# Kernel tuning notes

Hardware: AMD Instinct MI355X
Metric: run time of the kernel (lower is better)

Reference implementation:

```python
import jax, jax.numpy as jnp
import numpy as np

N = 100000      # nodes
E = 3200000     # edges
F_IN = 128      # num_features
H = 32          # hidden_dim (hard-coded in module)
C = 8           # num_classes
B = 128         # graphs in batch
BN_EPS = 1e-5


def setup_inputs() -> dict:
    key = jax.random.key(0)
    ks = jax.random.split(key, 24)
    s = 0.1
    inp = {
        "x": jax.random.normal(ks[0], (N, F_IN), jnp.float32),
        "edge_index": jax.random.randint(ks[1], (2, E), 0, N, dtype=jnp.int32),
        "batch": jnp.sort(jax.random.randint(ks[2], (N,), 0, B, dtype=jnp.int32)),
        # GINConv layer 0 (F_IN -> H -> H) MLP + BN params
        "w1_0": jax.random.normal(ks[3], (F_IN, H), jnp.float32) * s,
        "b1_0": jnp.zeros((H,), jnp.float32),
        "w2_0": jax.random.normal(ks[4], (H, H), jnp.float32) * s,
        "b2_0": jnp.zeros((H,), jnp.float32),
        "g_0": jnp.ones((H,), jnp.float32),
        "be_0": jnp.zeros((H,), jnp.float32),
        # GINConv layers 1..3 (H -> H -> H), stacked
        "w1s": jax.random.normal(ks[5], (3, H, H), jnp.float32) * s,
        "b1s": jnp.zeros((3, H), jnp.float32),
        "w2s": jax.random.normal(ks[6], (3, H, H), jnp.float32) * s,
        "b2s": jnp.zeros((3, H), jnp.float32),
        "gs": jnp.ones((3, H), jnp.float32),
        "bes": jnp.zeros((3, H), jnp.float32),
        # classifier head
        "fc1_w": jax.random.normal(ks[7], (H, H), jnp.float32) * s,
        "fc1_b": jnp.zeros((H,), jnp.float32),
        "fc2_w": jax.random.normal(ks[8], (H, C), jnp.float32) * s,
        "fc2_b": jnp.zeros((C,), jnp.float32),
    }
    return inp


def _gin_conv(h, src, dst, w1, b1, w2, b2):
    # GINConv with eps=0: MLP((1+eps)*x + sum_{j in N(i)} x_j)
    agg = jax.ops.segment_sum(h[src], dst, num_segments=N)  # scatter-add aggregation
    z = h + agg
    return jnp.maximum(z @ w1 + b1, 0.0) @ w2 + b2


def _batch_norm(h, gamma, beta):
    # BatchNorm1d in training mode: batch stats over node dim, biased variance
    mean = h.mean(axis=0)
    var = jnp.mean(jnp.square(h - mean), axis=0)
    return gamma * (h - mean) * jax.lax.rsqrt(var + BN_EPS) + beta


def reference(x, edge_index, batch, w1_0, b1_0, w2_0, b2_0, g_0, be_0,
              w1s, b1s, w2s, b2s, gs, bes, fc1_w, fc1_b, fc2_w, fc2_b):
    src, dst = edge_index[0], edge_index[1]
    h = _batch_norm(jnp.maximum(_gin_conv(x, src, dst, w1_0, b1_0, w2_0, b2_0), 0.0), g_0, be_0)
    for i in range(3):  # fixed small layer loop
        h = _batch_norm(jnp.maximum(_gin_conv(h, src, dst, w1s[i], b1s[i], w2s[i], b2s[i]), 0.0), gs[i], bes[i])
    # global_mean_pool over batch ids
    counts = jax.ops.segment_sum(jnp.ones((N,), h.dtype), batch, num_segments=B)
    pooled = jax.ops.segment_sum(h, batch, num_segments=B) / jnp.maximum(counts, 1.0)[:, None]
    h = jnp.maximum(pooled @ fc1_w + fc1_b, 0.0)
    # dropout p=0.5 treated as identity (eval-mode determinism)
    logits = h @ fc2_w + fc2_b
    return jax.nn.log_softmax(logits, axis=-1)
```

## Files before the change

### kernel.cpp

```cpp
#include <hip/hip_runtime.h>
#include <hip/hip_bf16.h>

#define NN   100000
#define EE   3200000
#define HH   32
#define BB   128
#define KMAX 96
#define LSTRIDE 97
#define NBKT 256
#define BSPAN 391
#define WSPAN 98
#define QS   25000
#define EBLK 256
#define CHUNK 12500

static constexpr size_t Q_OFF      = 0;
static constexpr size_t AGG_OFF    = 6400000;
static constexpr size_t H_OFF      = 19200000;
static constexpr size_t EPACK_OFF  = 32000000;
static constexpr size_t EPACK2_OFF = 44800000;
static constexpr size_t SRC_OFF    = 57600000;
static constexpr size_t OFF_OFF    = 70400000;
static constexpr size_t HIST_OFF   = 70900000;
static constexpr size_t START_OFF  = 71200000;
static constexpr size_t BBASE_OFF  = 71500000;
static constexpr size_t KB2_OFF    = 71510000;
static constexpr size_t STATS_OFF  = 71530000;
static constexpr size_t POOLED_OFF = 71531024;
static constexpr size_t PCNT_OFF   = 71547408;
static constexpr size_t ZERO_OFF   = STATS_OFF;
static constexpr size_t ZERO_BYTES = 17920;

__global__ __launch_bounds__(256) void hist_kernel(const int* __restrict__ ei,
                                                   int* __restrict__ hist) {
    __shared__ int lh[NBKT];
    int tid = threadIdx.x, blk = blockIdx.x;
    for (int i = tid; i < NBKT; i += 256) lh[i] = 0;
    __syncthreads();
    int e0 = blk * CHUNK;
    for (int e = e0 + tid; e < e0 + CHUNK; e += 256) {
        int d = ei[EE + e];
        atomicAdd(&lh[d / BSPAN], 1);
    }
    __syncthreads();
    for (int i = tid; i < NBKT; i += 256) hist[blk * NBKT + i] = lh[i];
}

__global__ __launch_bounds__(NBKT) void bucket_scan_kernel(const int* __restrict__ hist,
                                                           int* __restrict__ bbase,
                                                           int* __restrict__ start) {
    __shared__ int sm[NBKT];
    int t = threadIdx.x;
    int mine = 0;
    for (int blk = 0; blk < EBLK; blk++) mine += hist[blk * NBKT + t];
    sm[t] = mine;
    __syncthreads();
    for (int off = 1; off < NBKT; off <<= 1) {
        int v = (t >= off) ? sm[t - off] : 0;
        __syncthreads();
        sm[t] += v;
        __syncthreads();
    }
    int base = sm[t] - mine;
    bbase[t] = base;
    if (t == NBKT - 1) bbase[NBKT] = sm[t];
    int run = base;
    for (int blk = 0; blk < EBLK; blk++) {
        start[blk * NBKT + t] = run;
        run += hist[blk * NBKT + t];
    }
}

__global__ __launch_bounds__(256) void scatter_kernel(const int* __restrict__ ei,
                                                      const int* __restrict__ start,
                                                      int* __restrict__ epack) {
    __shared__ int loff[NBKT];
    int tid = threadIdx.x, blk = blockIdx.x;
    for (int i = tid; i < NBKT; i += 256) loff[i] = start[blk * NBKT + i];
    __syncthreads();
    int e0 = blk * CHUNK;
    for (int e = e0 + tid; e < e0 + CHUNK; e += 256) {
        int s = ei[e];
        int d = ei[EE + e];
        int b = d / BSPAN;
        int slot = atomicAdd(&loff[b], 1);
        epack[slot] = s | ((d - b * BSPAN) << 17);
    }
}

__global__ __launch_bounds__(256) void rescatter_kernel(const int* __restrict__ epack,
                                                        const int* __restrict__ bbase,
                                                        int* __restrict__ epack2,
                                                        int* __restrict__ kb2) {
    __shared__ int lh[16];
    __shared__ int lofs[17];
    __shared__ int lrun[16];
    int b = blockIdx.x, tid = threadIdx.x;
    if (tid < 16) lh[tid] = 0;
    __syncthreads();
    int p0 = bbase[b], p1 = bbase[b + 1];
    for (int i = p0 + tid; i < p1; i += 256) {
        int wd = epack[i];
        int key = ((wd >> 17) / WSPAN) * 4 + (wd & 0x1FFFF) / QS;
        atomicAdd(&lh[key], 1);
    }
    __syncthreads();
    if (tid == 0) {
        int run = p0;
        for (int k = 0; k < 16; k++) { lofs[k] = run; run += lh[k]; }
        lofs[16] = run;
    }
    __syncthreads();
    if (tid < 17) kb2[b * 17 + tid] = lofs[tid];
    if (tid < 16) lrun[tid] = lofs[tid];
    __syncthreads();
    for (int i = p0 + tid; i < p1; i += 256) {
        int wd = epack[i];
        int key = ((wd >> 17) / WSPAN) * 4 + (wd & 0x1FFFF) / QS;
        int slot = atomicAdd(&lrun[key], 1);
        epack2[slot] = wd;
    }
}

__global__ __launch_bounds__(256) void csr_compact_kernel(const int* __restrict__ epack2,
                                                          const int* __restrict__ kb2,
                                                          int* __restrict__ off,
                                                          int* __restrict__ srcs) {
    __shared__ int lcnt[WSPAN];
    __shared__ int lbase[WSPAN + 1];
    __shared__ int lcsr[WSPAN * LSTRIDE];
    int blk = blockIdx.x;
    int b = blk >> 2, w = blk & 3;
    int base = b * BSPAN;
    int span = NN - base;
    if (span <= 0) return;
    if (span > BSPAN) span = BSPAN;
    int wstart = w * WSPAN;
    if (wstart >= span) return;
    int wend = min(wstart + WSPAN, span);
    int wn = wend - wstart;
    int tid = threadIdx.x;
    for (int i = tid; i < wn; i += 256) lcnt[i] = 0;
    __syncthreads();
    int p0w = kb2[b * 17 + w * 4], p1w = kb2[b * 17 + w * 4 + 4];
    for (int i = p0w + tid; i < p1w; i += 256) {
        int wd = epack2[i];
        int ld = (wd >> 17) - wstart;
        int slot = atomicAdd(&lcnt[ld], 1);
        if (slot < KMAX) lcsr[ld * LSTRIDE + slot] = wd & 0x1FFFF;
    }
    __syncthreads();
    if (tid == 0) {
        int run = 0;
        for (int i = 0; i < wn; i++) { lbase[i] = run; run += min(lcnt[i], KMAX); }
        lbase[wn] = run;
    }
    __syncthreads();
    for (int i = tid; i < wn; i += 256) off[base + wstart + i] = p0w + lbase[i];
    if (base + wend == NN && tid == 0) off[NN] = p0w + lbase[wn];
    int m = lbase[wn];
    for (int j = tid; j < m; j += 256) {
        int lo = 0, hi = wn - 1;
        while (lo < hi) {
            int mid = (lo + hi + 1) >> 1;
            if (lbase[mid] <= j) lo = mid; else hi = mid - 1;
        }
        srcs[p0w + j] = lcsr[lo * LSTRIDE + (j - lbase[lo])];
    }
}

__device__ __forceinline__ unsigned bf16rn(float f) {
    unsigned b = __float_as_uint(f);
    return (b + 0x7fffu + ((b >> 16) & 1u)) >> 16;
}

__device__ __forceinline__ void acc_row(float* a, uint4 v) {
    a[0] += __uint_as_float(v.x << 16);
    a[1] += __uint_as_float(v.x & 0xffff0000u);
    a[2] += __uint_as_float(v.y << 16);
    a[3] += __uint_as_float(v.y & 0xffff0000u);
    a[4] += __uint_as_float(v.z << 16);
    a[5] += __uint_as_float(v.z & 0xffff0000u);
    a[6] += __uint_as_float(v.w << 16);
    a[7] += __uint_as_float(v.w & 0xffff0000u);
}

template <int FIN>
__global__ __launch_bounds__(256) void proj_kernel(const float* __restrict__ hin,
                                                   const float* __restrict__ w1,
                                                   const float* __restrict__ stats_prev,
                                                   const float* __restrict__ gamma,
                                                   const float* __restrict__ beta,
                                                   uint4* __restrict__ q4) {
    constexpr int JC = FIN / 4;
    __shared__ float sa[32], sc[32];
    __shared__ float part[4 * 64 * 33];
    int tid = threadIdx.x;
    if constexpr (FIN == 32) {
        if (tid < 32) {
            float mean = stats_prev[tid] * (1.0f / NN);
            float var  = fmaxf(stats_prev[32 + tid] * (1.0f / NN) - mean * mean, 0.f);
            float av = gamma[tid] * rsqrtf(var + 1e-5f);
            sa[tid] = av;
            sc[tid] = beta[tid] - mean * av;
        }
        __syncthreads();
    }
    int wv = __builtin_amdgcn_readfirstlane(tid >> 6);
    int ln = tid & 63;
    int n = blockIdx.x * 64 + ln;
    float acc[32];
#pragma unroll
    for (int c = 0; c < 32; c++) acc[c] = 0.f;
    if (n < NN) {
        const float4* h4 = (const float4*)(hin + (size_t)n * FIN + wv * JC);
        float hv[JC];
#pragma unroll
        for (int k = 0; k < JC / 4; k++) {
            float4 v = h4[k];
            hv[4*k] = v.x; hv[4*k+1] = v.y; hv[4*k+2] = v.z; hv[4*k+3] = v.w;
        }
        if constexpr (FIN == 32) {
#pragma unroll
            for (int j = 0; j < JC; j++) hv[j] = fmaf(hv[j], sa[wv * JC + j], sc[wv * JC + j]);
        }
#pragma unroll 4
        for (int j = 0; j < JC; j++) {
            float hvj = hv[j];
            const float* wrow = w1 + (size_t)(wv * JC + j) * 32;
#pragma unroll
            for (int c = 0; c < 32; c++) acc[c] = fmaf(hvj, wrow[c], acc[c]);
        }
    }
    float* my = part + (wv * 64 + ln) * 33;
#pragma unroll
    for (int c = 0; c < 32; c++) my[c] = acc[c];
    __syncthreads();
    int node = tid >> 2, p = tid & 3;
    int n2 = blockIdx.x * 64 + node;
    if (n2 >= NN) return;
    float r[8];
#pragma unroll
    for (int k = 0; k < 8; k++) {
        int c = p * 8 + k;
        r[k] = (part[(0 * 64 + node) * 33 + c] + part[(1 * 64 + node) * 33 + c])
             + (part[(2 * 64 + node) * 33 + c] + part[(3 * 64 + node) * 33 + c]);
    }
    uint4 u;
    u.x = bf16rn(r[0]) | (bf16rn(r[1]) << 16);
    u.y = bf16rn(r[2]) | (bf16rn(r[3]) << 16);
    u.z = bf16rn(r[4]) | (bf16rn(r[5]) << 16);
    u.w = bf16rn(r[6]) | (bf16rn(r[7]) << 16);
    q4[(size_t)n2 * 4 + p] = u;
}

__global__ __launch_bounds__(256) void gather_kernel(const uint4* __restrict__ q4,
                                                     const int* __restrict__ srcs,
                                                     const int* __restrict__ off,
                                                     const float* __restrict__ b1,
                                                     float* __restrict__ agg) {
    int t = blockIdx.x * 256 + threadIdx.x;
    int n = t >> 2;
    if (n >= NN) return;
    int p = t & 3;
    float a[8];
#pragma unroll
    for (int k = 0; k < 8; k++) a[k] = b1[p * 8 + k];
    acc_row(a, q4[(size_t)n * 4 + p]);
    int o0 = off[n];
    int d = off[n + 1] - o0;
    const int* lst = srcs + o0;
    int i = 0;
    for (; i + 8 <= d; i += 8) {
        int s0 = __builtin_nontemporal_load(lst + i);
        int s1 = __builtin_nontemporal_load(lst + i + 1);
        int s2 = __builtin_nontemporal_load(lst + i + 2);
        int s3 = __builtin_nontemporal_load(lst + i + 3);
        int s4 = __builtin_nontemporal_load(lst + i + 4);
        int s5 = __builtin_nontemporal_load(lst + i + 5);
        int s6 = __builtin_nontemporal_load(lst + i + 6);
        int s7 = __builtin_nontemporal_load(lst + i + 7);
        uint4 v0 = q4[(size_t)s0 * 4 + p];
        uint4 v1 = q4[(size_t)s1 * 4 + p];
        uint4 v2 = q4[(size_t)s2 * 4 + p];
        uint4 v3 = q4[(size_t)s3 * 4 + p];
        uint4 v4 = q4[(size_t)s4 * 4 + p];
        uint4 v5 = q4[(size_t)s5 * 4 + p];
        uint4 v6 = q4[(size_t)s6 * 4 + p];
        uint4 v7 = q4[(size_t)s7 * 4 + p];
        acc_row(a, v0); acc_row(a, v1); acc_row(a, v2); acc_row(a, v3);
        acc_row(a, v4); acc_row(a, v5); acc_row(a, v6); acc_row(a, v7);
    }
    for (; i < d; i++) {
        int s = __builtin_nontemporal_load(lst + i);
        acc_row(a, q4[(size_t)s * 4 + p]);
    }
    float4* ar = (float4*)(agg + (size_t)n * 32 + p * 8);
    float4 f0, f1;
    f0.x = a[0]; f0.y = a[1]; f0.z = a[2]; f0.w = a[3];
    f1.x = a[4]; f1.y = a[5]; f1.z = a[6]; f1.w = a[7];
    ar[0] = f0; ar[1] = f1;
}

__global__ __launch_bounds__(256) void mlp_kernel(const float* __restrict__ agg,
                                                  const float* __restrict__ w2,
                                                  const float* __restrict__ b2,
                                                  float* __restrict__ r,
                                                  float* __restrict__ stats) {
    __shared__ float tile[256 * 33];
    __shared__ float ps[8 * 32];
    __shared__ float pq[8 * 32];
    int tid = threadIdx.x;
    int n = blockIdx.x * 256 + tid;
    float rc[32];
    if (n < NN) {
        float u[32];
        const float4* a4 = (const float4*)(agg + (size_t)n * 32);
#pragma unroll
        for (int k = 0; k < 8; k++) {
            float4 v = a4[k];
            u[4*k]   = fmaxf(v.x, 0.f);
            u[4*k+1] = fmaxf(v.y, 0.f);
            u[4*k+2] = fmaxf(v.z, 0.f);
            u[4*k+3] = fmaxf(v.w, 0.f);
        }
#pragma unroll
        for (int c = 0; c < 32; c++) rc[c] = b2[c];
#pragma unroll 4
        for (int j = 0; j < 32; j++) {
            float uj = u[j];
            const float* wrow = w2 + (size_t)j * 32;
#pragma unroll
            for (int c = 0; c < 32; c++) rc[c] = fmaf(uj, wrow[c], rc[c]);
        }
#pragma unroll
        for (int c = 0; c < 32; c++) rc[c] = fmaxf(rc[c], 0.f);
        float4* rr = (float4*)(r + (size_t)n * 32);
#pragma unroll
        for (int k = 0; k < 8; k++) {
            float4 v; v.x = rc[4*k]; v.y = rc[4*k+1]; v.z = rc[4*k+2]; v.w = rc[4*k+3];
            rr[k] = v;
        }
    } else {
#pragma unroll
        for (int c = 0; c < 32; c++) rc[c] = 0.f;
    }
#pragma unroll
    for (int c = 0; c < 32; c++) tile[tid * 33 + c] = rc[c];
    __syncthreads();
    {
        int c = tid & 31, rb = tid >> 5;
        float s = 0.f, sq = 0.f;
        for (int it = 0; it < 32; it++) {
            float v = tile[(rb * 32 + it) * 33 + c];
            s += v; sq += v * v;
        }
        ps[rb * 32 + c] = s; pq[rb * 32 + c] = sq;
    }
    __syncthreads();
    if (tid < 32) {
        float s = 0.f, sq = 0.f;
#pragma unroll
        for (int rb = 0; rb < 8; rb++) { s += ps[rb * 32 + tid]; sq += pq[rb * 32 + tid]; }
        atomicAdd(&stats[tid], s);
        atomicAdd(&stats[32 + tid], sq);
    }
}

#define PR 16
__global__ __launch_bounds__(256) void pool_kernel(const float* __restrict__ h,
                                                   const int* __restrict__ batch,
                                                   float* __restrict__ pooled,
                                                   float* __restrict__ pcnt) {
    int t = blockIdx.x * 256 + threadIdx.x;
    int c = t & 31;
    int g = t >> 5;
    int r0 = g * PR;
    if (r0 >= NN) return;
    int r1 = min(r0 + PR, NN);
    int cur = batch[r0];
    float acc = 0.f, cn = 0.f;
    for (int rr = r0; rr < r1; rr++) {
        int b = batch[rr];
        if (b != cur) {
            atomicAdd(&pooled[cur * 32 + c], acc);
            if (c == 0) atomicAdd(&pcnt[cur], cn);
            acc = 0.f; cn = 0.f; cur = b;
        }
        acc += h[(size_t)rr * 32 + c];
        cn += 1.f;
    }
    atomicAdd(&pooled[cur * 32 + c], acc);
    if (c == 0) atomicAdd(&pcnt[cur], cn);
}

__global__ __launch_bounds__(128) void head_kernel(const float* __restrict__ pooled,
                                                   const float* __restrict__ pcnt,
                                                   const float* __restrict__ stats3,
                                                   const float* __restrict__ g3,
                                                   const float* __restrict__ be3,
                                                   const float* __restrict__ fc1w,
                                                   const float* __restrict__ fc1b,
                                                   const float* __restrict__ fc2w,
                                                   const float* __restrict__ fc2b,
                                                   float* __restrict__ out) {
    __shared__ float sa[32], sc[32];
    int g = threadIdx.x;
    if (g < 32) {
        float mean = stats3[g] * (1.0f / NN);
        float var  = fmaxf(stats3[32 + g] * (1.0f / NN) - mean * mean, 0.f);
        float av = g3[g] * rsqrtf(var + 1e-5f);
        sa[g] = av;
        sc[g] = be3[g] - mean * av;
    }
    __syncthreads();
    if (g >= BB) return;
    float inv = 1.f / fmaxf(pcnt[g], 1.f);
    float xv[32];
#pragma unroll
    for (int c = 0; c < 32; c++) xv[c] = fmaf(sa[c], pooled[g * 32 + c] * inv, sc[c]);
    float u[32];
#pragma unroll 4
    for (int k = 0; k < 32; k++) {
        float s = fc1b[k];
#pragma unroll
        for (int c = 0; c < 32; c++) s = fmaf(xv[c], fc1w[c * 32 + k], s);
        u[k] = fmaxf(s, 0.f);
    }
    float l[8];
#pragma unroll
    for (int o = 0; o < 8; o++) {
        float s = fc2b[o];
#pragma unroll
        for (int k = 0; k < 32; k++) s = fmaf(u[k], fc2w[k * 8 + o], s);
        l[o] = s;
    }
    float m = l[0];
#pragma unroll
    for (int o = 1; o < 8; o++) m = fmaxf(m, l[o]);
    float se = 0.f;
#pragma unroll
    for (int o = 0; o < 8; o++) se += expf(l[o] - m);
    float lse = logf(se) + m;
#pragma unroll
    for (int o = 0; o < 8; o++) out[g * 8 + o] = l[o] - lse;
}

extern "C" void kernel_launch(void* const* d_in, const int* in_sizes, int n_in,
                              void* d_out, int out_size, void* d_ws, size_t ws_size,
                              hipStream_t stream) {
    const float* x    = (const float*)d_in[0];
    const int*   ei   = (const int*)d_in[1];
    const int*   batch= (const int*)d_in[2];
    const float* w1_0 = (const float*)d_in[3];
    const float* b1_0 = (const float*)d_in[4];
    const float* w2_0 = (const float*)d_in[5];
    const float* b2_0 = (const float*)d_in[6];
    const float* g_0  = (const float*)d_in[7];
    const float* be_0 = (const float*)d_in[8];
    const float* w1s  = (const float*)d_in[9];
    const float* b1s  = (const float*)d_in[10];
    const float* w2s  = (const float*)d_in[11];
    const float* b2s  = (const float*)d_in[12];
    const float* gs   = (const float*)d_in[13];
    const float* bes  = (const float*)d_in[14];
    const float* fc1w = (const float*)d_in[15];
    const float* fc1b = (const float*)d_in[16];
    const float* fc2w = (const float*)d_in[17];
    const float* fc2b = (const float*)d_in[18];
    float* out = (float*)d_out;

    char* ws = (char*)d_ws;
    uint4*    q4     = (uint4*)(ws + Q_OFF);
    float*    agg    = (float*)(ws + AGG_OFF);
    float*    h      = (float*)(ws + H_OFF);
    int*      epack  = (int*)(ws + EPACK_OFF);
    int*      epack2 = (int*)(ws + EPACK2_OFF);
    int*      srcs   = (int*)(ws + SRC_OFF);
    int*      off    = (int*)(ws + OFF_OFF);
    int*      hist   = (int*)(ws + HIST_OFF);
    int*      start  = (int*)(ws + START_OFF);
    int*      bbase  = (int*)(ws + BBASE_OFF);
    int*      kb2    = (int*)(ws + KB2_OFF);
    float*    stats  = (float*)(ws + STATS_OFF);
    float*    pooled = (float*)(ws + POOLED_OFF);
    float*    pcnt   = (float*)(ws + PCNT_OFF);

    (void)hipMemsetAsync(ws + ZERO_OFF, 0, ZERO_BYTES, stream);

    hist_kernel<<<EBLK, 256, 0, stream>>>(ei, hist);
    bucket_scan_kernel<<<1, NBKT, 0, stream>>>(hist, bbase, start);
    scatter_kernel<<<EBLK, 256, 0, stream>>>(ei, start, epack);
    rescatter_kernel<<<NBKT, 256, 0, stream>>>(epack, bbase, epack2, kb2);
    csr_compact_kernel<<<NBKT * 4, 256, 0, stream>>>(epack2, kb2, off, srcs);

    const int pblk = (NN + 63) / 64;
    const int nblk = (NN + 255) / 256;
    const int gblk = (NN * 4 + 255) / 256;

    proj_kernel<128><<<pblk, 256, 0, stream>>>(x, w1_0, nullptr, nullptr, nullptr, q4);
    gather_kernel<<<gblk, 256, 0, stream>>>(q4, srcs, off, b1_0, agg);
    mlp_kernel<<<nblk, 256, 0, stream>>>(agg, w2_0, b2_0, h, stats);

    for (int i = 0; i < 3; i++) {
        const float* st_prev = stats + i * 64;
        proj_kernel<32><<<pblk, 256, 0, stream>>>(h, w1s + i * 1024, st_prev,
                                                  gs + i * 32, bes + i * 32, q4);
        gather_kernel<<<gblk, 256, 0, stream>>>(q4, srcs, off, b1s + i * 32, agg);
        mlp_kernel<<<nblk, 256, 0, stream>>>(agg, w2s + i * 1024, b2s + i * 32, h,
                                             stats + (i + 1) * 64);
    }

    int pthreads = ((NN + PR - 1) / PR) * 32;
    pool_kernel<<<(pthreads + 255) / 256, 256, 0, stream>>>(h, batch, pooled, pcnt);
    head_kernel<<<1, 128, 0, stream>>>(pooled, pcnt, stats + 3 * 64, gs + 2 * 32,
                                       bes + 2 * 32, fc1w, fc1b, fc2w, fc2b, out);
}
```

Baseline: 595.0 us.

## Split MLP second layer across four threads per node with shuffle-based stats

The per-node second MLP layer now spreads each node over four threads, each computing eight output channels. The full input row is assembled with wave shuffles, and W2 is staged transposed in shared memory. BatchNorm statistics are reduced with xor shuffles and shared atomics instead of a padded 256x33 shared tile. This aims to raise occupancy and coalescing and to cut shared-memory traffic, at the cost of extra shuffles and four times as many blocks each reloading W2.

New measurement: 756.9 us. 1.27x slower.

```diff
diff --git a/kernel.cpp b/kernel.cpp
--- a/kernel.cpp
+++ b/kernel.cpp
@@ -302,69 +302,89 @@
     ar[0] = f0; ar[1] = f1;
 }
 
-__global__ __launch_bounds__(256) void mlp_kernel(const float* __restrict__ agg,
-                                                  const float* __restrict__ w2,
-                                                  const float* __restrict__ b2,
-                                                  float* __restrict__ r,
-                                                  float* __restrict__ stats) {
-    __shared__ float tile[256 * 33];
-    __shared__ float ps[8 * 32];
-    __shared__ float pq[8 * 32];
+__global__ __launch_bounds__(256) void mlp2_kernel(const float* __restrict__ agg,
+                                                   const float* __restrict__ w2,
+                                                   const float* __restrict__ b2,
+                                                   float* __restrict__ hout,
+                                                   float* __restrict__ stats) {
+    __shared__ float w2t[32 * 33];
+    __shared__ float sacc[64];
     int tid = threadIdx.x;
-    int n = blockIdx.x * 256 + tid;
-    float rc[32];
+    for (int i = tid; i < 1024; i += 256) w2t[(i & 31) * 33 + (i >> 5)] = w2[i];
+    if (tid < 64) sacc[tid] = 0.f;
+    __syncthreads();
+    int t = blockIdx.x * 256 + tid;
+    int n = t >> 2;
+    int p = t & 3;
+    float r[8];
+#pragma unroll
+    for (int k = 0; k < 8; k++) r[k] = 0.f;
     if (n < NN) {
-        float u[32];
-        const float4* a4 = (const float4*)(agg + (size_t)n * 32);
-#pragma unroll
-        for (int k = 0; k < 8; k++) {
-            float4 v = a4[k];
-            u[4*k]   = fmaxf(v.x, 0.f);
-            u[4*k+1] = fmaxf(v.y, 0.f);
-            u[4*k+2] = fmaxf(v.z, 0.f);
-            u[4*k+3] = fmaxf(v.w, 0.f);
-        }
-#pragma unroll
-        for (int c = 0; c < 32; c++) rc[c] = b2[c];
+        const float4* a4 = (const float4*)(agg + (size_t)n * 32 + p * 8);
+        float4 z0 = a4[0], z1 = a4[1];
+        float um[8];
+        um[0] = fmaxf(z0.x, 0.f); um[1] = fmaxf(z0.y, 0.f);
+        um[2] = fmaxf(z0.z, 0.f); um[3] = fmaxf(z0.w, 0.f);
+        um[4] = fmaxf(z1.x, 0.f); um[5] = fmaxf(z1.y, 0.f);
+        um[6] = fmaxf(z1.z, 0.f); um[7] = fmaxf(z1.w, 0.f);
+        float u16[16];
+        {
+            int half = p & 1;
+#pragma unroll
+            for (int k = 0; k < 8; k++) {
+                float o = __shfl_xor(um[k], 1);
+                u16[half * 8 + k] = um[k];
+                u16[(half ^ 1) * 8 + k] = o;
+            }
+        }
+        float u32v[32];
+        {
+            int halfq = (p >> 1) & 1;
+#pragma unroll
+            for (int k = 0; k < 16; k++) {
+                float o = __shfl_xor(u16[k], 2);
+                u32v[halfq * 16 + k] = u16[k];
+                u32v[(halfq ^ 1) * 16 + k] = o;
+            }
+        }
+        float v[8];
+#pragma unroll
+        for (int k = 0; k < 8; k++) v[k] = b2[p * 8 + k];
 #pragma unroll 4
         for (int j = 0; j < 32; j++) {
-            float uj = u[j];
-            const float* wrow = w2 + (size_t)j * 32;
-#pragma unroll
-            for (int c = 0; c < 32; c++) rc[c] = fmaf(uj, wrow[c], rc[c]);
-        }
-#pragma unroll
-        for (int c = 0; c < 32; c++) rc[c] = fmaxf(rc[c], 0.f);
-        float4* rr = (float4*)(r + (size_t)n * 32);
+            float uj = u32v[j];
+#pragma unroll
+            for (int k = 0; k < 8; k++)
+                v[k] = fmaf(uj, w2t[(p * 8 + k) * 33 + j], v[k]);
+        }
+#pragma unroll
+        for (int k = 0; k < 8; k++) r[k] = fmaxf(v[k], 0.f);
+        float4* hr = (float4*)(hout + (size_t)n * 32 + p * 8);
+        float4 f0, f1;
+        f0.x = r[0]; f0.y = r[1]; f0.z = r[2]; f0.w = r[3];
+        f1.x = r[4]; f1.y = r[5]; f1.z = r[6]; f1.w = r[7];
+        hr[0] = f0; hr[1] = f1;
+    }
+    float s[8], sq[8];
+#pragma unroll
+    for (int k = 0; k < 8; k++) { s[k] = r[k]; sq[k] = r[k] * r[k]; }
+#pragma unroll
+    for (int m = 4; m < 64; m <<= 1) {
 #pragma unroll
         for (int k = 0; k < 8; k++) {
-            float4 v; v.x = rc[4*k]; v.y = rc[4*k+1]; v.z = rc[4*k+2]; v.w = rc[4*k+3];
-            rr[k] = v;
-        }
-    } else {
-#pragma unroll
-        for (int c = 0; c < 32; c++) rc[c] = 0.f;
-    }
-#pragma unroll
-    for (int c = 0; c < 32; c++) tile[tid * 33 + c] = rc[c];
-    __syncthreads();
-    {
-        int c = tid & 31, rb = tid >> 5;
-        float s = 0.f, sq = 0.f;
-        for (int it = 0; it < 32; it++) {
-            float v = tile[(rb * 32 + it) * 33 + c];
-            s += v; sq += v * v;
-        }
-        ps[rb * 32 + c] = s; pq[rb * 32 + c] = sq;
-    }
-    __syncthreads();
-    if (tid < 32) {
-        float s = 0.f, sq = 0.f;
-#pragma unroll
-        for (int rb = 0; rb < 8; rb++) { s += ps[rb * 32 + tid]; sq += pq[rb * 32 + tid]; }
-        atomicAdd(&stats[tid], s);
-        atomicAdd(&stats[32 + tid], sq);
-    }
+            s[k]  += __shfl_xor(s[k], m);
+            sq[k] += __shfl_xor(sq[k], m);
+        }
+    }
+    if (((tid & 63) >> 2) == 0) {
+#pragma unroll
+        for (int k = 0; k < 8; k++) {
+            atomicAdd(&sacc[p * 8 + k], s[k]);
+            atomicAdd(&sacc[32 + p * 8 + k], sq[k]);
+        }
+    }
+    __syncthreads();
+    if (tid < 64) atomicAdd(&stats[tid], sacc[tid]);
 }
 
 #define PR 16
@@ -495,20 +515,20 @@
     csr_compact_kernel<<<NBKT * 4, 256, 0, stream>>>(epack2, kb2, off, srcs);
 
     const int pblk = (NN + 63) / 64;
-    const int nblk = (NN + 255) / 256;
     const int gblk = (NN * 4 + 255) / 256;
+    const int mblk = (NN * 4 + 255) / 256;
 
     proj_kernel<128><<<pblk, 256, 0, stream>>>(x, w1_0, nullptr, nullptr, nullptr, q4);
     gather_kernel<<<gblk, 256, 0, stream>>>(q4, srcs, off, b1_0, agg);
-    mlp_kernel<<<nblk, 256, 0, stream>>>(agg, w2_0, b2_0, h, stats);
+    mlp2_kernel<<<mblk, 256, 0, stream>>>(agg, w2_0, b2_0, h, stats);
 
     for (int i = 0; i < 3; i++) {
         const float* st_prev = stats + i * 64;
         proj_kernel<32><<<pblk, 256, 0, stream>>>(h, w1s + i * 1024, st_prev,
                                                   gs + i * 32, bes + i * 32, q4);
         gather_kernel<<<gblk, 256, 0, stream>>>(q4, srcs, off, b1s + i * 32, agg);
-        mlp_kernel<<<nblk, 256, 0, stream>>>(agg, w2s + i * 1024, b2s + i * 32, h,
-                                             stats + (i + 1) * 64);
+        mlp2_kernel<<<mblk, 256, 0, stream>>>(agg, w2s + i * 1024, b2s + i * 32, h,
+                                              stats + (i + 1) * 64);
     }
 
     int pthreads = ((NN + PR - 1) / PR) * 32;
```
